# Kernel tuning notes

Hardware: AMD Instinct MI355X
Metric: run time of the kernel (lower is better)

The kernel has to match this reference:

```python
import jax, jax.numpy as jnp
import numpy as np

N = 10000
E = 160000
IN_C = 512
OUT_C = 1024
NEG_SLOPE = 0.2


def setup_inputs() -> dict:
    key = jax.random.key(0)
    ks = jax.random.split(key, 12)
    x = jax.random.normal(ks[0], (N, IN_C), dtype=jnp.float32)
    edge_index = jax.random.randint(ks[1], (2, E), 0, N, dtype=jnp.int32)
    s_in = 1.0 / np.sqrt(IN_C)
    s_out = 1.0 / np.sqrt(OUT_C)
    return {
        "x": x,
        "edge_index": edge_index,
        "W1": jax.random.normal(ks[2], (IN_C, OUT_C), dtype=jnp.float32) * s_in,
        "a_src1": jax.random.normal(ks[3], (OUT_C,), dtype=jnp.float32) * s_out,
        "a_dst1": jax.random.normal(ks[4], (OUT_C,), dtype=jnp.float32) * s_out,
        "b1": jnp.zeros((OUT_C,), dtype=jnp.float32),
        "W2": jax.random.normal(ks[5], (IN_C, OUT_C), dtype=jnp.float32) * s_in,
        "a_src2": jax.random.normal(ks[6], (OUT_C,), dtype=jnp.float32) * s_out,
        "a_dst2": jax.random.normal(ks[7], (OUT_C,), dtype=jnp.float32) * s_out,
        "b2": jnp.zeros((OUT_C,), dtype=jnp.float32),
        "prelu_a": jnp.asarray(0.25, dtype=jnp.float32),
        "Wp1": jax.random.normal(ks[8], (OUT_C, OUT_C), dtype=jnp.float32) * s_out,
        "bp1": jnp.zeros((OUT_C,), dtype=jnp.float32),
        "Wp2": jax.random.normal(ks[9], (OUT_C, 1024), dtype=jnp.float32) * s_out,
    }


def _gat_conv(x, src, dst, W, a_src, a_dst, b):
    # x: [N, in], W: [in, out]. PyG GATConv, heads=1, self-loops already in src/dst.
    h = x @ W  # [N, out]
    alpha_s = h @ a_src  # [N]
    alpha_d = h @ a_dst  # [N]
    e = alpha_s[src] + alpha_d[dst]  # [E+N]
    e = jnp.where(e >= 0, e, NEG_SLOPE * e)  # LeakyReLU(0.2)
    # segment softmax over destination nodes
    m = jax.ops.segment_max(e, dst, num_segments=N)  # [N]
    ex = jnp.exp(e - m[dst])
    denom = jax.ops.segment_sum(ex, dst, num_segments=N)  # [N], >=1 via self-loops
    alpha = ex / denom[dst]  # [E+N]
    out = jax.ops.segment_sum(alpha[:, None] * h[src], dst, num_segments=N)
    return out + b


def reference(x, edge_index, W1, a_src1, a_dst1, b1, W2, a_src2, a_dst2, b2,
              prelu_a, Wp1, bp1, Wp2):
    # add self loops (PyG GATConv default)
    loops = jnp.arange(N, dtype=edge_index.dtype)
    src = jnp.concatenate([edge_index[0], loops])
    dst = jnp.concatenate([edge_index[1], loops])

    def prelu(v):
        return jnp.where(v >= 0, v, prelu_a * v)

    h1 = prelu(_gat_conv(x, src, dst, W1, a_src1, a_dst1, b1))  # [N, 1024]
    h2 = prelu(_gat_conv(x, src, dst, W2, a_src2, a_dst2, b2))  # [N, 1024]
    h = h1 + h2

    # semantic attention: project -> mean over nodes -> softmax over 1024 dims
    w = jnp.tanh(h @ Wp1 + bp1) @ Wp2  # [N, 1024]
    w = w.mean(axis=0)  # [1024]
    att = jax.nn.softmax(w, axis=0)  # [1024] == beta.mean(0).squeeze()
    return att * h1 + (1.0 - att) * h2
```

## Files before the change

### kernel.cpp

```cpp
#include <hip/hip_runtime.h>

#define IN_C 512
#define OUT_C 1024
#define NC2 2048
#define NEG_SLOPE 0.2f

typedef short frag8 __attribute__((ext_vector_type(8)));
typedef float f32x4 __attribute__((ext_vector_type(4)));

#define GLOAD_LDS16(g, l) __builtin_amdgcn_global_load_lds(\
    (const __attribute__((address_space(1))) void*)(g), \
    (__attribute__((address_space(3))) void*)(l), 16, 0, 0)

__device__ __forceinline__ unsigned short f2b(float f){
  unsigned u = __float_as_uint(f);
  unsigned r = (u + 0x7fffu + ((u >> 16) & 1u)) >> 16;
  return (unsigned short)r;
}
__device__ __forceinline__ float leaky(float v){ return v >= 0.f ? v : NEG_SLOPE * v; }


__global__ void prep_kernel(const float* __restrict__ W1, const float* __restrict__ W2,
                            const float* __restrict__ Wp1,
                            const float* __restrict__ a_src1, const float* __restrict__ a_dst1,
                            const float* __restrict__ a_src2, const float* __restrict__ a_dst2,
                            unsigned short* __restrict__ WT, unsigned short* __restrict__ Wp1T,
                            float* __restrict__ uv, int* __restrict__ counts,
                            int* __restrict__ cursor, int N){
  __shared__ float tile[32][33];
  int b = blockIdx.x;
  int tx = threadIdx.x & 31, ty = threadIdx.x >> 5;
  if (b < 1024){
    const float* in = (b >> 9) ? W2 : W1;
    int rowOff = (b >> 9) * OUT_C;
    int bb = b & 511;
    int c0 = (bb & 31) * 32, r0 = (bb >> 5) * 32;
    for (int i = ty; i < 32; i += 8)
      tile[i][tx] = in[(size_t)(r0 + i) * OUT_C + c0 + tx];
    __syncthreads();
    for (int i = ty; i < 32; i += 8)
      WT[(size_t)(c0 + i + rowOff) * IN_C + r0 + tx] = f2b(tile[tx][i]);
  } else if (b < 2048){
    int bb = b - 1024;
    int c0 = (bb & 31) * 32, r0 = (bb >> 5) * 32;
    for (int i = ty; i < 32; i += 8)
      tile[i][tx] = Wp1[(size_t)(r0 + i) * OUT_C + c0 + tx];
    __syncthreads();
    for (int i = ty; i < 32; i += 8)
      Wp1T[(size_t)(c0 + i) * OUT_C + r0 + tx] = f2b(tile[tx][i]);
  } else if (b < 2560){
    int g = (b - 2048) * 4 + (threadIdx.x >> 6);
    int lane = threadIdx.x & 63;
    int which = g >> 9;
    int i = g & 511;
    const float* W = (which < 2) ? W1 : W2;
    const float* a = (which == 0) ? a_src1 : (which == 1) ? a_dst1 : (which == 2) ? a_src2 : a_dst2;
    const float* row = W + (size_t)i * OUT_C;
    float s = 0.f;
    for (int j = lane; j < OUT_C; j += 64) s += row[j] * a[j];
    for (int off = 32; off; off >>= 1) s += __shfl_down(s, off);
    if (lane == 0) uv[which * IN_C + i] = s;
  } else {
    int i = (b - 2560) * 256 + threadIdx.x;
    if (i < N){ counts[i] = 0; cursor[i] = 0; }
  }
}


__global__ void alphahist_kernel(const float* __restrict__ x, const float* __restrict__ uv,
                                 const int* __restrict__ dst,
                                 unsigned short* __restrict__ xb,
                                 float2* __restrict__ sa, float2* __restrict__ da,
                                 float2* __restrict__ ese,
                                 int* __restrict__ counts,
                                 float* __restrict__ colsum, float* __restrict__ wv,
                                 int N, int E){
  int b = blockIdx.x;
  if (b >= N){
    int e = (b - N) * 256 + threadIdx.x;
    if (e < E) atomicAdd(&counts[dst[e]], 1);
    return;
  }
  int n = b;
  int w = threadIdx.x >> 6, lane = threadIdx.x & 63;
  __shared__ float sh[4];
  if (n < 8){
    int i = n * 256 + threadIdx.x;
    if (i < 1024) colsum[i] = 0.f; else wv[i - 1024] = 0.f;
  }
  const float4* rv = (const float4*)(x + (size_t)n * IN_C);
  const float4* un = (const float4*)(uv + w * IN_C);
  float4 v0 = rv[lane], v1 = rv[lane + 64];
  float4 u0 = un[lane], u1 = un[lane + 64];
  float s = v0.x*u0.x + v0.y*u0.y + v0.z*u0.z + v0.w*u0.w
          + v1.x*u1.x + v1.y*u1.y + v1.z*u1.z + v1.w*u1.w;
  if (w == 0){
    ushort4 p0, p1;
    p0.x = f2b(v0.x); p0.y = f2b(v0.y); p0.z = f2b(v0.z); p0.w = f2b(v0.w);
    p1.x = f2b(v1.x); p1.y = f2b(v1.y); p1.z = f2b(v1.z); p1.w = f2b(v1.w);
    *(ushort4*)(xb + (size_t)n * IN_C + lane * 4) = p0;
    *(ushort4*)(xb + (size_t)n * IN_C + 256 + lane * 4) = p1;
  }
  for (int off = 32; off; off >>= 1) s += __shfl_down(s, off);
  if (lane == 0) sh[w] = s;
  __syncthreads();
  if (threadIdx.x == 0){
    float2 vsa; vsa.x = sh[0]; vsa.y = sh[2];
    float2 vda; vda.x = sh[1]; vda.y = sh[3];
    sa[n] = vsa; da[n] = vda;
    float2 es;
    es.x = expf(leaky(sh[0] + sh[1]));
    es.y = expf(leaky(sh[2] + sh[3]));
    ese[n] = es;
  }
}


__global__ __launch_bounds__(1024) void scan_kernel(const int* __restrict__ counts,
                                                    int* __restrict__ offs, int n){
  __shared__ int ws[16];
  __shared__ int base_s;
  int tid = threadIdx.x, lane = tid & 63, wave = tid >> 6;
  if (tid == 0) base_s = 0;
  __syncthreads();
  for (int base = 0; base < n; base += 1024){
    int i = base + tid;
    int v = (i < n) ? counts[i] : 0;
    int sc = v;
    for (int o = 1; o < 64; o <<= 1){
      int t = __shfl_up(sc, o);
      if (lane >= o) sc += t;
    }
    if (lane == 63) ws[wave] = sc;
    __syncthreads();
    int wp = 0, tot = 0;
#pragma unroll
    for (int k = 0; k < 16; k++){ int w_ = ws[k]; if (k < wave) wp += w_; tot += w_; }
    if (i < n) offs[i] = base_s + wp + sc - v;
    __syncthreads();
    if (tid == 0) base_s += tot;
    __syncthreads();
  }
}


__global__ void csr_kernel(const int* __restrict__ src, const int* __restrict__ dst,
                           const int* __restrict__ offs, int* cursor,
                           int* __restrict__ nsrc, int E){
  int e = blockIdx.x * 256 + threadIdx.x;
  if (e >= E) return;
  int d = dst[e];
  int p = atomicAdd(&cursor[d], 1);
  nsrc[offs[d] + p] = src[e];
}


#define AGG_FMA8(ACC, W, U) \
  ACC[0] += (W) * __uint_as_float(((unsigned)(U).x) << 16); \
  ACC[1] += (W) * __uint_as_float(((unsigned)(U).x) & 0xffff0000u); \
  ACC[2] += (W) * __uint_as_float(((unsigned)(U).y) << 16); \
  ACC[3] += (W) * __uint_as_float(((unsigned)(U).y) & 0xffff0000u); \
  ACC[4] += (W) * __uint_as_float(((unsigned)(U).z) << 16); \
  ACC[5] += (W) * __uint_as_float(((unsigned)(U).z) & 0xffff0000u); \
  ACC[6] += (W) * __uint_as_float(((unsigned)(U).w) << 16); \
  ACC[7] += (W) * __uint_as_float(((unsigned)(U).w) & 0xffff0000u);

__global__ __launch_bounds__(256) void aggx_kernel(
    const int* __restrict__ counts, const int* __restrict__ offs,
    const int* __restrict__ nsrc,
    const float2* __restrict__ sa, const float2* __restrict__ da,
    const float2* __restrict__ ese,
    const unsigned short* __restrict__ xb,
    unsigned short* __restrict__ xa1b, unsigned short* __restrict__ xa2b, int N){
  int wid = threadIdx.x >> 6, lane = threadIdx.x & 63;
  int d = blockIdx.x * 4 + wid;
  if (d >= N) return;
  float2 dad = da[d];
  int deg = counts[d], off = offs[d];
  float acc1[8] = {0,0,0,0,0,0,0,0}, acc2[8] = {0,0,0,0,0,0,0,0};
  float den1 = 0.f, den2 = 0.f;
  const unsigned short* Xb = xb + lane * 8;
  for (int base = 0; base < deg; base += 64){
    int i = base + lane;
    int s = 0; float x1 = 0.f, x2 = 0.f;
    if (i < deg){
      s = nsrc[off + i];
      float2 sas = sa[s];
      x1 = expf(leaky(sas.x + dad.x));
      x2 = expf(leaky(sas.y + dad.y));
    }
    den1 += x1; den2 += x2;
    int cnt = min(64, deg - base);
#pragma unroll 4
    for (int j = 0; j < cnt; j++){
      int sj = __shfl(s, j);
      float w1j = __shfl(x1, j);
      float w2j = __shfl(x2, j);
      int4 u = *(const int4*)(Xb + (size_t)sj * IN_C);
      AGG_FMA8(acc1, w1j, u)
      AGG_FMA8(acc2, w2j, u)
    }
  }
  for (int o = 32; o; o >>= 1){
    den1 += __shfl_xor(den1, o);
    den2 += __shfl_xor(den2, o);
  }
  float2 es = ese[d];
  {
    int4 u = *(const int4*)(Xb + (size_t)d * IN_C);
    AGG_FMA8(acc1, es.x, u)
    AGG_FMA8(acc2, es.y, u)
  }
  den1 += es.x; den2 += es.y;
  float inv1 = 1.f / den1, inv2 = 1.f / den2;
  size_t outb = (size_t)d * IN_C + lane * 8;
  int4 o1, o2;
  o1.x = (int)((unsigned)f2b(acc1[0]*inv1) | ((unsigned)f2b(acc1[1]*inv1) << 16));
  o1.y = (int)((unsigned)f2b(acc1[2]*inv1) | ((unsigned)f2b(acc1[3]*inv1) << 16));
  o1.z = (int)((unsigned)f2b(acc1[4]*inv1) | ((unsigned)f2b(acc1[5]*inv1) << 16));
  o1.w = (int)((unsigned)f2b(acc1[6]*inv1) | ((unsigned)f2b(acc1[7]*inv1) << 16));
  o2.x = (int)((unsigned)f2b(acc2[0]*inv2) | ((unsigned)f2b(acc2[1]*inv2) << 16));
  o2.y = (int)((unsigned)f2b(acc2[2]*inv2) | ((unsigned)f2b(acc2[3]*inv2) << 16));
  o2.z = (int)((unsigned)f2b(acc2[4]*inv2) | ((unsigned)f2b(acc2[5]*inv2) << 16));
  o2.w = (int)((unsigned)f2b(acc2[6]*inv2) | ((unsigned)f2b(acc2[7]*inv2) << 16));
  *(int4*)(xa1b + outb) = o1;
  *(int4*)(xa2b + outb) = o2;
}


__global__ __launch_bounds__(256) void gemmh_kernel(const unsigned short* __restrict__ A1,
                                                    const unsigned short* __restrict__ A2,
                                                    const unsigned short* __restrict__ BT,
                                                    const float* __restrict__ b1,
                                                    const float* __restrict__ b2,
                                                    const float* __restrict__ prelu_a,
                                                    unsigned short* __restrict__ hsum,
                                                    unsigned short* __restrict__ hdiff,
                                                    int M, int Mtiles, int perx){
  const int bid = blockIdx.x;
  const int xcd = bid & 7;
  const int li = bid >> 3;
  const int bn_t = li & 7;
  const int bm_t = xcd * perx + (li >> 3);
  if (bm_t >= Mtiles) return;
  const int bm = bm_t * 64, bn = bn_t * 128;
  __shared__ unsigned short Al[64 * 32];
  __shared__ unsigned short Bl[128 * 32];
  const int t = threadIdx.x;
  const int lane = t & 63, wid = t >> 6;
  const int wj = wid;
  const int l16 = lane & 15, q = lane >> 4;
  const int lch = (lane & 3) * 8;
  f32x4 acc1[4][2] = {};
  f32x4 acc2[4][2] = {};
  const int arow = bm + wid * 16 + (lane >> 2);
  const int brow0 = bn + wid * 32 + (lane >> 2);
  const int ga = min(arow, M - 1);
  const unsigned short* pa1 = A1 + (size_t)ga * IN_C + lch;
  const unsigned short* pa2 = A2 + (size_t)ga * IN_C + lch;
  const unsigned short* pb0 = BT + (size_t)brow0 * IN_C + lch;
  const unsigned short* pb1 = BT + (size_t)(brow0 + 16) * IN_C + lch;
  const size_t boff2 = (size_t)OUT_C * IN_C;
  for (int k0 = 0; k0 < IN_C; k0 += 32){
    GLOAD_LDS16(pa1 + k0, &Al[(wid * 16) * 32]);
    GLOAD_LDS16(pb0 + k0, &Bl[(wid * 32) * 32]);
    GLOAD_LDS16(pb1 + k0, &Bl[(wid * 32 + 16) * 32]);
    __syncthreads();
    frag8 af[4], bf[2];
#pragma unroll
    for (int mi = 0; mi < 4; mi++) af[mi] = *(const frag8*)&Al[(mi*16 + l16) * 32 + q*8];
#pragma unroll
    for (int nj = 0; nj < 2; nj++) bf[nj] = *(const frag8*)&Bl[(wj*32 + nj*16 + l16) * 32 + q*8];
#pragma unroll
    for (int mi = 0; mi < 4; mi++)
#pragma unroll
      for (int nj = 0; nj < 2; nj++)
        acc1[mi][nj] = __builtin_amdgcn_mfma_f32_16x16x32_bf16(af[mi], bf[nj], acc1[mi][nj], 0, 0, 0);
    __syncthreads();
  }
  for (int k0 = 0; k0 < IN_C; k0 += 32){
    GLOAD_LDS16(pa2 + k0, &Al[(wid * 16) * 32]);
    GLOAD_LDS16(pb0 + boff2 + k0, &Bl[(wid * 32) * 32]);
    GLOAD_LDS16(pb1 + boff2 + k0, &Bl[(wid * 32 + 16) * 32]);
    __syncthreads();
    frag8 af[4], bf[2];
#pragma unroll
    for (int mi = 0; mi < 4; mi++) af[mi] = *(const frag8*)&Al[(mi*16 + l16) * 32 + q*8];
#pragma unroll
    for (int nj = 0; nj < 2; nj++) bf[nj] = *(const frag8*)&Bl[(wj*32 + nj*16 + l16) * 32 + q*8];
#pragma unroll
    for (int mi = 0; mi < 4; mi++)
#pragma unroll
      for (int nj = 0; nj < 2; nj++)
        acc2[mi][nj] = __builtin_amdgcn_mfma_f32_16x16x32_bf16(af[mi], bf[nj], acc2[mi][nj], 0, 0, 0);
    __syncthreads();
  }
  float pa = prelu_a[0];
#pragma unroll
  for (int mi = 0; mi < 4; mi++){
#pragma unroll
    for (int r = 0; r < 4; r++){
      int row = bm + mi*16 + q*4 + r;
      if (row >= M) continue;
#pragma unroll
      for (int nj = 0; nj < 2; nj++){
        int col = bn + wj*32 + nj*16 + l16;
        float v1 = acc1[mi][nj][r] + b1[col];
        v1 = v1 >= 0.f ? v1 : pa * v1;
        float v2 = acc2[mi][nj][r] + b2[col];
        v2 = v2 >= 0.f ? v2 : pa * v2;
        size_t idx = (size_t)row * OUT_C + col;
        hsum[idx]  = f2b(v1 + v2);
        hdiff[idx] = f2b(v1 - v2);
      }
    }
  }
}


__global__ __launch_bounds__(256) void gemm2_kernel(const unsigned short* __restrict__ A,
                                                    const unsigned short* __restrict__ BT,
                                                    const float* __restrict__ bp1,
                                                    float* __restrict__ colsum,
                                                    int M, int Mtiles, int perx){
  const int bid = blockIdx.x;
  const int xcd = bid & 7;
  const int li = bid >> 3;
  const int bn_t = li & 7;
  const int bm_t = xcd * perx + (li >> 3);
  if (bm_t >= Mtiles) return;
  const int bm = bm_t * 64, bn = bn_t * 128;
  __shared__ unsigned short Al[64 * 32];
  __shared__ unsigned short Bl[128 * 32];
  __shared__ float cs[128];
  const int t = threadIdx.x;
  const int lane = t & 63, wid = t >> 6;
  const int wj = wid;
  const int l16 = lane & 15, q = lane >> 4;
  const int lch = (lane & 3) * 8;
  if (t < 128) cs[t] = 0.f;
  f32x4 acc[4][2] = {};
  const int arow = bm + wid * 16 + (lane >> 2);
  const int brow0 = bn + wid * 32 + (lane >> 2);
  const int ga = min(arow, M - 1);
  const unsigned short* pa = A + (size_t)ga * OUT_C + lch;
  const unsigned short* pb0 = BT + (size_t)brow0 * OUT_C + lch;
  const unsigned short* pb1 = BT + (size_t)(brow0 + 16) * OUT_C + lch;
  for (int k0 = 0; k0 < OUT_C; k0 += 32){
    GLOAD_LDS16(pa + k0, &Al[(wid * 16) * 32]);
    GLOAD_LDS16(pb0 + k0, &Bl[(wid * 32) * 32]);
    GLOAD_LDS16(pb1 + k0, &Bl[(wid * 32 + 16) * 32]);
    __syncthreads();
    frag8 af[4], bf[2];
#pragma unroll
    for (int mi = 0; mi < 4; mi++) af[mi] = *(const frag8*)&Al[(mi*16 + l16) * 32 + q*8];
#pragma unroll
    for (int nj = 0; nj < 2; nj++) bf[nj] = *(const frag8*)&Bl[(wj*32 + nj*16 + l16) * 32 + q*8];
#pragma unroll
    for (int mi = 0; mi < 4; mi++)
#pragma unroll
      for (int nj = 0; nj < 2; nj++)
        acc[mi][nj] = __builtin_amdgcn_mfma_f32_16x16x32_bf16(af[mi], bf[nj], acc[mi][nj], 0, 0, 0);
    __syncthreads();
  }
#pragma unroll
  for (int nj = 0; nj < 2; nj++){
    int col = bn + wj*32 + nj*16 + l16;
    float bias = bp1[col];
    float p = 0.f;
#pragma unroll
    for (int mi = 0; mi < 4; mi++){
#pragma unroll
      for (int r = 0; r < 4; r++){
        int row = bm + mi*16 + q*4 + r;
        float tv = tanhf(acc[mi][nj][r] + bias);
        if (row < M) p += tv;
      }
    }
    p += __shfl_xor(p, 16);
    p += __shfl_xor(p, 32);
    if (q == 0) atomicAdd(&cs[wj*32 + nj*16 + l16], p);
  }
  __syncthreads();
  if (t < 128) atomicAdd(&colsum[bn + t], cs[t]);
}


__global__ void wproj_kernel(const float* __restrict__ colsum, const float* __restrict__ Wp2,
                             float* __restrict__ wv){
  int o = blockIdx.x * 256 + threadIdx.x;
  int c0 = blockIdx.y * 128;
  float acc = 0.f;
  for (int c = c0; c < c0 + 128; c++) acc += colsum[c] * Wp2[(size_t)c * OUT_C + o];
  atomicAdd(&wv[o], acc);
}

__global__ __launch_bounds__(1024) void softmax_kernel(const float* __restrict__ wv,
                                                       float* __restrict__ att, float invN){
  int o = threadIdx.x;
  __shared__ float red[1024];
  float w = wv[o] * invN;
  red[o] = w; __syncthreads();
  for (int s = 512; s > 0; s >>= 1){ if (o < s) red[o] = fmaxf(red[o], red[o + s]); __syncthreads(); }
  float m = red[0]; __syncthreads();
  float e = expf(w - m);
  red[o] = e; __syncthreads();
  for (int s = 512; s > 0; s >>= 1){ if (o < s) red[o] += red[o + s]; __syncthreads(); }
  att[o] = e / red[0];
}

__global__ void combine_kernel(const float* __restrict__ att, const unsigned short* __restrict__ hs,
                               const unsigned short* __restrict__ hd, float* __restrict__ out, int total8){
  int i = blockIdx.x * 256 + threadIdx.x;
  if (i >= total8) return;
  int colb = (i & 127) * 8;
  int4 us = ((const int4*)hs)[i];
  int4 ud = ((const int4*)hd)[i];
  float4 a0 = *(const float4*)(att + colb);
  float4 a1 = *(const float4*)(att + colb + 4);
  float o[8]; float sv, dv;
  sv = __uint_as_float(((unsigned)us.x) << 16);        dv = __uint_as_float(((unsigned)ud.x) << 16);
  o[0] = 0.5f * sv + (a0.x - 0.5f) * dv;
  sv = __uint_as_float(((unsigned)us.x) & 0xffff0000u); dv = __uint_as_float(((unsigned)ud.x) & 0xffff0000u);
  o[1] = 0.5f * sv + (a0.y - 0.5f) * dv;
  sv = __uint_as_float(((unsigned)us.y) << 16);        dv = __uint_as_float(((unsigned)ud.y) << 16);
  o[2] = 0.5f * sv + (a0.z - 0.5f) * dv;
  sv = __uint_as_float(((unsigned)us.y) & 0xffff0000u); dv = __uint_as_float(((unsigned)ud.y) & 0xffff0000u);
  o[3] = 0.5f * sv + (a0.w - 0.5f) * dv;
  sv = __uint_as_float(((unsigned)us.z) << 16);        dv = __uint_as_float(((unsigned)ud.z) << 16);
  o[4] = 0.5f * sv + (a1.x - 0.5f) * dv;
  sv = __uint_as_float(((unsigned)us.z) & 0xffff0000u); dv = __uint_as_float(((unsigned)ud.z) & 0xffff0000u);
  o[5] = 0.5f * sv + (a1.y - 0.5f) * dv;
  sv = __uint_as_float(((unsigned)us.w) << 16);        dv = __uint_as_float(((unsigned)ud.w) << 16);
  o[6] = 0.5f * sv + (a1.z - 0.5f) * dv;
  sv = __uint_as_float(((unsigned)us.w) & 0xffff0000u); dv = __uint_as_float(((unsigned)ud.w) & 0xffff0000u);
  o[7] = 0.5f * sv + (a1.w - 0.5f) * dv;
  float4 f0; f0.x = o[0]; f0.y = o[1]; f0.z = o[2]; f0.w = o[3];
  float4 f1; f1.x = o[4]; f1.y = o[5]; f1.z = o[6]; f1.w = o[7];
  *(float4*)(out + (size_t)i * 8) = f0;
  *(float4*)(out + (size_t)i * 8 + 4) = f1;
}


extern "C" void kernel_launch(void* const* d_in, const int* in_sizes, int n_in,
                              void* d_out, int out_size, void* d_ws, size_t ws_size,
                              hipStream_t stream){
  const float* x      = (const float*)d_in[0];
  const int*   edge   = (const int*)d_in[1];
  const float* W1     = (const float*)d_in[2];
  const float* a_src1 = (const float*)d_in[3];
  const float* a_dst1 = (const float*)d_in[4];
  const float* b1     = (const float*)d_in[5];
  const float* W2     = (const float*)d_in[6];
  const float* a_src2 = (const float*)d_in[7];
  const float* a_dst2 = (const float*)d_in[8];
  const float* b2     = (const float*)d_in[9];
  const float* prelu_a= (const float*)d_in[10];
  const float* Wp1    = (const float*)d_in[11];
  const float* bp1    = (const float*)d_in[12];
  const float* Wp2    = (const float*)d_in[13];
  const int N = in_sizes[0] / IN_C;
  const int E = in_sizes[1] / 2;
  const int* srcArr = edge;
  const int* dstArr = edge + E;

  char* ws = (char*)d_ws;
  size_t o = 0;
  auto alloc = [&](size_t b) -> char* {
    char* p = ws + o;
    o = (o + b + 255) & ~(size_t)255;
    return p;
  };
  unsigned short* xb    = (unsigned short*)alloc((size_t)N * IN_C * 2);
  unsigned short* WT    = (unsigned short*)alloc((size_t)NC2 * IN_C * 2);
  unsigned short* Wp1T  = (unsigned short*)alloc((size_t)OUT_C * OUT_C * 2);
  unsigned short* xa1b  = (unsigned short*)alloc((size_t)N * IN_C * 2);
  unsigned short* xa2b  = (unsigned short*)alloc((size_t)N * IN_C * 2);
  unsigned short* hsum  = (unsigned short*)alloc((size_t)N * OUT_C * 2);
  unsigned short* hdiff = (unsigned short*)alloc((size_t)N * OUT_C * 2);
  float*          uv    = (float*)alloc(4 * IN_C * 4);
  float2*         sa    = (float2*)alloc((size_t)N * 8);
  float2*         da    = (float2*)alloc((size_t)N * 8);
  float2*         ese   = (float2*)alloc((size_t)N * 8);
  int*            counts= (int*)alloc((size_t)N * 4);
  int*            offs  = (int*)alloc((size_t)(N + 1) * 4);
  int*            cursor= (int*)alloc((size_t)N * 4);
  int*            nsrc  = (int*)alloc((size_t)E * 4);
  float*          colsum= (float*)alloc(OUT_C * 4);
  float*          wv    = (float*)alloc(OUT_C * 4);
  float*          att   = (float*)alloc(OUT_C * 4);

  const int Mtiles = (N + 63) / 64;
  const int perx = (Mtiles + 7) / 8;
  const int gemmgrid = 8 * perx * 8;
  const int zblocks = (N + 255) / 256;
  const int eblocks = (E + 255) / 256;

  prep_kernel<<<2560 + zblocks, 256, 0, stream>>>(W1, W2, Wp1, a_src1, a_dst1, a_src2, a_dst2,
                                                  WT, Wp1T, uv, counts, cursor, N);
  alphahist_kernel<<<N + eblocks, 256, 0, stream>>>(x, uv, dstArr, xb, sa, da, ese,
                                                    counts, colsum, wv, N, E);
  scan_kernel<<<1, 1024, 0, stream>>>(counts, offs, N);
  csr_kernel<<<eblocks, 256, 0, stream>>>(srcArr, dstArr, offs, cursor, nsrc, E);
  aggx_kernel<<<(N + 3) / 4, 256, 0, stream>>>(counts, offs, nsrc, sa, da, ese,
                                               xb, xa1b, xa2b, N);
  gemmh_kernel<<<gemmgrid, 256, 0, stream>>>(xa1b, xa2b, WT, b1, b2, prelu_a,
                                             hsum, hdiff, N, Mtiles, perx);
  gemm2_kernel<<<gemmgrid, 256, 0, stream>>>(hsum, Wp1T, bp1, colsum, N, Mtiles, perx);
  wproj_kernel<<<dim3(4, 8), 256, 0, stream>>>(colsum, Wp2, wv);
  softmax_kernel<<<1, 1024, 0, stream>>>(wv, att, 1.0f / (float)N);
  combine_kernel<<<(N * OUT_C / 8 + 255) / 256, 256, 0, stream>>>(att, hsum, hdiff, (float*)d_out,
                                                                  N * OUT_C / 8);
}
```

Baseline: 279.9 us.

## Fuse scan with CSR build and wproj with softmax to cut launches

Merges the scan and CSR-fill kernels into one launch: block 0 does the prefix scan and publishes a flag, and the other blocks spin on it before scattering edges. The wproj and softmax kernels are also merged, with a last-block-done counter so the final block computes the softmax. The histogram work is folded into the alphahist node blocks rather than extra blocks. The goal is to remove kernel launch gaps and tiny serial kernels. The spin-wait depends on block 0 being scheduled alongside the waiting blocks (157 blocks, which should fit), and the aggx FMA macro is rewritten as a loop with no change in behaviour.

```diff
diff --git a/kernel.cpp b/kernel.cpp
--- a/kernel.cpp
+++ b/kernel.cpp
@@ -26,7 +26,7 @@
                             const float* __restrict__ a_src2, const float* __restrict__ a_dst2,
                             unsigned short* __restrict__ WT, unsigned short* __restrict__ Wp1T,
                             float* __restrict__ uv, int* __restrict__ counts,
-                            int* __restrict__ cursor, int N){
+                            int* __restrict__ cursor, int* __restrict__ ctrl, int N){
   __shared__ float tile[32][33];
   int b = blockIdx.x;
   int tx = threadIdx.x & 31, ty = threadIdx.x >> 5;
@@ -63,6 +63,7 @@
   } else {
     int i = (b - 2560) * 256 + threadIdx.x;
     if (i < N){ counts[i] = 0; cursor[i] = 0; }
+    if (b == 2560 && threadIdx.x < 2) ctrl[threadIdx.x] = 0;
   }
 }
 
@@ -75,13 +76,12 @@
                                  int* __restrict__ counts,
                                  float* __restrict__ colsum, float* __restrict__ wv,
                                  int N, int E){
-  int b = blockIdx.x;
-  if (b >= N){
-    int e = (b - N) * 256 + threadIdx.x;
+  int n = blockIdx.x;
+  int eblocks = (E + 255) / 256;
+  for (int c = n; c < eblocks; c += N){
+    int e = c * 256 + threadIdx.x;
     if (e < E) atomicAdd(&counts[dst[e]], 1);
-    return;
-  }
-  int n = b;
+  }
   int w = threadIdx.x >> 6, lane = threadIdx.x & 63;
   __shared__ float sh[4];
   if (n < 8){
@@ -116,54 +116,53 @@
 }
 
 
-__global__ __launch_bounds__(1024) void scan_kernel(const int* __restrict__ counts,
-                                                    int* __restrict__ offs, int n){
-  __shared__ int ws[16];
-  __shared__ int base_s;
+__global__ __launch_bounds__(1024) void scancsr_kernel(const int* __restrict__ counts,
+                                                       int* __restrict__ offs,
+                                                       const int* __restrict__ src,
+                                                       const int* __restrict__ dst,
+                                                       int* cursor, int* __restrict__ nsrc,
+                                                       int* ctrl, int N, int E){
   int tid = threadIdx.x, lane = tid & 63, wave = tid >> 6;
-  if (tid == 0) base_s = 0;
+  if (blockIdx.x == 0){
+    __shared__ int ws[16];
+    __shared__ int base_s;
+    if (tid == 0) base_s = 0;
+    __syncthreads();
+    for (int base = 0; base < N; base += 1024){
+      int i = base + tid;
+      int v = (i < N) ? counts[i] : 0;
+      int sc = v;
+      for (int o = 1; o < 64; o <<= 1){
+        int t = __shfl_up(sc, o);
+        if (lane >= o) sc += t;
+      }
+      if (lane == 63) ws[wave] = sc;
+      __syncthreads();
+      int wp = 0, tot = 0;
+#pragma unroll
+      for (int k = 0; k < 16; k++){ int w_ = ws[k]; if (k < wave) wp += w_; tot += w_; }
+      if (i < N) offs[i] = base_s + wp + sc - v;
+      __syncthreads();
+      if (tid == 0) base_s += tot;
+      __syncthreads();
+    }
+    if (tid == 0){
+      __threadfence();
+      __hip_atomic_store(&ctrl[0], 1, __ATOMIC_RELEASE, __HIP_MEMORY_SCOPE_AGENT);
+    }
+  }
+  if (tid == 0){
+    while (__hip_atomic_load(&ctrl[0], __ATOMIC_ACQUIRE, __HIP_MEMORY_SCOPE_AGENT) == 0){}
+  }
   __syncthreads();
-  for (int base = 0; base < n; base += 1024){
-    int i = base + tid;
-    int v = (i < n) ? counts[i] : 0;
-    int sc = v;
-    for (int o = 1; o < 64; o <<= 1){
-      int t = __shfl_up(sc, o);
-      if (lane >= o) sc += t;
-    }
-    if (lane == 63) ws[wave] = sc;
-    __syncthreads();
-    int wp = 0, tot = 0;
-#pragma unroll
-    for (int k = 0; k < 16; k++){ int w_ = ws[k]; if (k < wave) wp += w_; tot += w_; }
-    if (i < n) offs[i] = base_s + wp + sc - v;
-    __syncthreads();
-    if (tid == 0) base_s += tot;
-    __syncthreads();
-  }
-}
-
-
-__global__ void csr_kernel(const int* __restrict__ src, const int* __restrict__ dst,
-                           const int* __restrict__ offs, int* cursor,
-                           int* __restrict__ nsrc, int E){
-  int e = blockIdx.x * 256 + threadIdx.x;
-  if (e >= E) return;
-  int d = dst[e];
-  int p = atomicAdd(&cursor[d], 1);
-  nsrc[offs[d] + p] = src[e];
-}
-
-
-#define AGG_FMA8(ACC, W, U) \
-  ACC[0] += (W) * __uint_as_float(((unsigned)(U).x) << 16); \
-  ACC[1] += (W) * __uint_as_float(((unsigned)(U).x) & 0xffff0000u); \
-  ACC[2] += (W) * __uint_as_float(((unsigned)(U).y) << 16); \
-  ACC[3] += (W) * __uint_as_float(((unsigned)(U).y) & 0xffff0000u); \
-  ACC[4] += (W) * __uint_as_float(((unsigned)(U).z) << 16); \
-  ACC[5] += (W) * __uint_as_float(((unsigned)(U).z) & 0xffff0000u); \
-  ACC[6] += (W) * __uint_as_float(((unsigned)(U).w) << 16); \
-  ACC[7] += (W) * __uint_as_float(((unsigned)(U).w) & 0xffff0000u);
+  int e = blockIdx.x * 1024 + tid;
+  if (e < E){
+    int d = dst[e];
+    int p = atomicAdd(&cursor[d], 1);
+    nsrc[offs[d] + p] = src[e];
+  }
+}
+
 
 __global__ __launch_bounds__(256) void aggx_kernel(
     const int* __restrict__ counts, const int* __restrict__ offs,
@@ -197,8 +196,17 @@
       float w1j = __shfl(x1, j);
       float w2j = __shfl(x2, j);
       int4 u = *(const int4*)(Xb + (size_t)sj * IN_C);
-      AGG_FMA8(acc1, w1j, u)
-      AGG_FMA8(acc2, w2j, u)
+      float f[8];
+      f[0] = __uint_as_float(((unsigned)u.x) << 16);
+      f[1] = __uint_as_float(((unsigned)u.x) & 0xffff0000u);
+      f[2] = __uint_as_float(((unsigned)u.y) << 16);
+      f[3] = __uint_as_float(((unsigned)u.y) & 0xffff0000u);
+      f[4] = __uint_as_float(((unsigned)u.z) << 16);
+      f[5] = __uint_as_float(((unsigned)u.z) & 0xffff0000u);
+      f[6] = __uint_as_float(((unsigned)u.w) << 16);
+      f[7] = __uint_as_float(((unsigned)u.w) & 0xffff0000u);
+#pragma unroll
+      for (int c = 0; c < 8; c++){ acc1[c] += w1j * f[c]; acc2[c] += w2j * f[c]; }
     }
   }
   for (int o = 32; o; o >>= 1){
@@ -208,8 +216,17 @@
   float2 es = ese[d];
   {
     int4 u = *(const int4*)(Xb + (size_t)d * IN_C);
-    AGG_FMA8(acc1, es.x, u)
-    AGG_FMA8(acc2, es.y, u)
+    float f[8];
+    f[0] = __uint_as_float(((unsigned)u.x) << 16);
+    f[1] = __uint_as_float(((unsigned)u.x) & 0xffff0000u);
+    f[2] = __uint_as_float(((unsigned)u.y) << 16);
+    f[3] = __uint_as_float(((unsigned)u.y) & 0xffff0000u);
+    f[4] = __uint_as_float(((unsigned)u.z) << 16);
+    f[5] = __uint_as_float(((unsigned)u.z) & 0xffff0000u);
+    f[6] = __uint_as_float(((unsigned)u.w) << 16);
+    f[7] = __uint_as_float(((unsigned)u.w) & 0xffff0000u);
+#pragma unroll
+    for (int c = 0; c < 8; c++){ acc1[c] += es.x * f[c]; acc2[c] += es.y * f[c]; }
   }
   den1 += es.x; den2 += es.y;
   float inv1 = 1.f / den1, inv2 = 1.f / den2;
@@ -386,27 +403,34 @@
 }
 
 
-__global__ void wproj_kernel(const float* __restrict__ colsum, const float* __restrict__ Wp2,
-                             float* __restrict__ wv){
+__global__ void wprojsm_kernel(const float* __restrict__ colsum, const float* __restrict__ Wp2,
+                               float* __restrict__ wv, float* __restrict__ att,
+                               int* ctrl, float invN){
   int o = blockIdx.x * 256 + threadIdx.x;
   int c0 = blockIdx.y * 128;
   float acc = 0.f;
   for (int c = c0; c < c0 + 128; c++) acc += colsum[c] * Wp2[(size_t)c * OUT_C + o];
   atomicAdd(&wv[o], acc);
-}
-
-__global__ __launch_bounds__(1024) void softmax_kernel(const float* __restrict__ wv,
-                                                       float* __restrict__ att, float invN){
-  int o = threadIdx.x;
-  __shared__ float red[1024];
-  float w = wv[o] * invN;
-  red[o] = w; __syncthreads();
-  for (int s = 512; s > 0; s >>= 1){ if (o < s) red[o] = fmaxf(red[o], red[o + s]); __syncthreads(); }
-  float m = red[0]; __syncthreads();
-  float e = expf(w - m);
-  red[o] = e; __syncthreads();
-  for (int s = 512; s > 0; s >>= 1){ if (o < s) red[o] += red[o + s]; __syncthreads(); }
-  att[o] = e / red[0];
+  __threadfence();
+  __shared__ int amlast;
+  __shared__ float red[256];
+  if (threadIdx.x == 0)
+    amlast = (atomicAdd(&ctrl[1], 1) == gridDim.x * gridDim.y - 1) ? 1 : 0;
+  __syncthreads();
+  if (!amlast) return;
+  __threadfence();
+  int t = threadIdx.x;
+  float w0 = wv[t] * invN, w1 = wv[t + 256] * invN,
+        w2 = wv[t + 512] * invN, w3 = wv[t + 768] * invN;
+  float m = fmaxf(fmaxf(w0, w1), fmaxf(w2, w3));
+  red[t] = m; __syncthreads();
+  for (int s = 128; s > 0; s >>= 1){ if (t < s) red[t] = fmaxf(red[t], red[t + s]); __syncthreads(); }
+  m = red[0]; __syncthreads();
+  float e0 = expf(w0 - m), e1 = expf(w1 - m), e2 = expf(w2 - m), e3 = expf(w3 - m);
+  red[t] = e0 + e1 + e2 + e3; __syncthreads();
+  for (int s = 128; s > 0; s >>= 1){ if (t < s) red[t] += red[t + s]; __syncthreads(); }
+  float inv = 1.f / red[0];
+  att[t] = e0 * inv; att[t + 256] = e1 * inv; att[t + 512] = e2 * inv; att[t + 768] = e3 * inv;
 }
 
 __global__ void combine_kernel(const float* __restrict__ att, const unsigned short* __restrict__ hs,
@@ -485,6 +509,7 @@
   int*            counts= (int*)alloc((size_t)N * 4);
   int*            offs  = (int*)alloc((size_t)(N + 1) * 4);
   int*            cursor= (int*)alloc((size_t)N * 4);
+  int*            ctrl  = (int*)alloc(2 * 4);
   int*            nsrc  = (int*)alloc((size_t)E * 4);
   float*          colsum= (float*)alloc(OUT_C * 4);
   float*          wv    = (float*)alloc(OUT_C * 4);
@@ -494,21 +519,20 @@
   const int perx = (Mtiles + 7) / 8;
   const int gemmgrid = 8 * perx * 8;
   const int zblocks = (N + 255) / 256;
-  const int eblocks = (E + 255) / 256;
+  const int sblocks = (E + 1023) / 1024;
 
   prep_kernel<<<2560 + zblocks, 256, 0, stream>>>(W1, W2, Wp1, a_src1, a_dst1, a_src2, a_dst2,
-                                                  WT, Wp1T, uv, counts, cursor, N);
-  alphahist_kernel<<<N + eblocks, 256, 0, stream>>>(x, uv, dstArr, xb, sa, da, ese,
-                                                    counts, colsum, wv, N, E);
-  scan_kernel<<<1, 1024, 0, stream>>>(counts, offs, N);
-  csr_kernel<<<eblocks, 256, 0, stream>>>(srcArr, dstArr, offs, cursor, nsrc, E);
+                                                  WT, Wp1T, uv, counts, cursor, ctrl, N);
+  alphahist_kernel<<<N, 256, 0, stream>>>(x, uv, dstArr, xb, sa, da, ese,
+                                          counts, colsum, wv, N, E);
+  scancsr_kernel<<<sblocks, 1024, 0, stream>>>(counts, offs, srcArr, dstArr, cursor, nsrc,
+                                               ctrl, N, E);
   aggx_kernel<<<(N + 3) / 4, 256, 0, stream>>>(counts, offs, nsrc, sa, da, ese,
                                                xb, xa1b, xa2b, N);
   gemmh_kernel<<<gemmgrid, 256, 0, stream>>>(xa1b, xa2b, WT, b1, b2, prelu_a,
                                              hsum, hdiff, N, Mtiles, perx);
   gemm2_kernel<<<gemmgrid, 256, 0, stream>>>(hsum, Wp1T, bp1, colsum, N, Mtiles, perx);
-  wproj_kernel<<<dim3(4, 8), 256, 0, stream>>>(colsum, Wp2, wv);
-  softmax_kernel<<<1, 1024, 0, stream>>>(wv, att, 1.0f / (float)N);
+  wprojsm_kernel<<<dim3(4, 8), 256, 0, stream>>>(colsum, Wp2, wv, att, ctrl, 1.0f / (float)N);
   combine_kernel<<<(N * OUT_C / 8 + 255) / 256, 256, 0, stream>>>(att, hsum, hdiff, (float*)d_out,
                                                                   N * OUT_C / 8);
 }
```

New measurement: 286.5 us. 1.02x slower.
